# Kernel optimization log

Measured on AMD Instinct MI355X. Metric: run time of the kernel, lower is better.

## Reference

```python
import jax, jax.numpy as jnp
import numpy as np

EPS = 1e-06
M = 10.0
IGNORE_LABEL = 100  # setup guarantees no label == 100, so the torch filter is a no-op


def setup_inputs() -> dict:
    key = jax.random.key(0)
    kf, kl = jax.random.split(key)
    n, d = 8192, 128
    features = jax.random.normal(kf, (n, d), dtype=jnp.float32)
    labels = jax.random.randint(kl, (n,), 0, 16, dtype=jnp.int64)
    return {"features": features, "labels": labels}


def reference(features, labels):
    # features: (n, d) float; labels: (n,) int, none equal to IGNORE_LABEL
    n = features.shape[0]
    dt = features.dtype

    # pairwise squared euclidean distances via Gram trick (avoids (n,n,d) tensor)
    sq = jnp.sum(features * features, axis=1)              # (n,)
    ed = sq[:, None] + sq[None, :] - 2.0 * (features @ features.T)  # (n, n)

    eq = labels[:, None] == labels[None, :]                # (n, n), includes diagonal
    counts = jnp.sum(eq, axis=1, keepdims=True).astype(dt) - 1.0  # (n, 1)

    eqf = eq.astype(dt)
    w = eqf / (counts + EPS) - (1.0 - eqf) / (n - counts - 1.0 + EPS)
    w = w * (1.0 - jnp.eye(n, dtype=dt))                   # zero diagonal

    loss = jnp.sum(w * ed, axis=1) + M                     # (n,)
    valid = (counts[:, 0] != 0.0).astype(dt)               # rows with same-class neighbors
    return jnp.sum(jax.nn.relu(loss) * valid) / jnp.maximum(jnp.sum(valid), 1.0)
```

## Files before the change

kernel.cpp:

```cpp
#include <hip/hip_runtime.h>

#define NCLASS 16
#define D 128
#define EPSF 1e-6f
#define MF 10.0f

#define WS_S   0
#define WS_Q   (NCLASS * D)
#define WS_CNT (WS_Q + NCLASS)
#define WS_SUM (WS_CNT + NCLASS)
#define WS_DONE 2082
#define WS_FLOATS 2084

#define AGG_BLOCKS 64
#define AGG_THREADS 512
#define AGG_WAVES (AGG_THREADS / 64)

__global__ void __launch_bounds__(AGG_THREADS)
agg_kernel(const float* __restrict__ F, const int* __restrict__ L,
           float* __restrict__ ws, int n) {
    __shared__ float Ssh[AGG_WAVES][NCLASS][D];
    __shared__ float qsh[AGG_WAVES][NCLASS];
    __shared__ float csh[AGG_WAVES][NCLASS];
    const int tid  = threadIdx.x;
    const int lane = tid & 63;
    const int wv   = tid >> 6;
    const int gw   = blockIdx.x * AGG_WAVES + wv;
    const int nwv  = AGG_BLOCKS * AGG_WAVES;

    float ax[NCLASS], ay[NCLASS], qa[NCLASS], ca[NCLASS];
    #pragma unroll
    for (int c = 0; c < NCLASS; ++c) { ax[c] = ay[c] = qa[c] = ca[c] = 0.f; }

    const float2* __restrict__ F2 = (const float2*)F;
    #pragma unroll 4
    for (int r = gw; r < n; r += nwv) {
        const int lc = L[r];
        const float2 v = F2[(size_t)r * 64 + lane];
        const float sq = fmaf(v.x, v.x, v.y * v.y);
        #pragma unroll
        for (int c = 0; c < NCLASS; ++c) {
            const float sel = (lc == c) ? 1.f : 0.f;
            ax[c] = fmaf(sel, v.x, ax[c]);
            ay[c] = fmaf(sel, v.y, ay[c]);
            qa[c] = fmaf(sel, sq, qa[c]);
            ca[c] += sel;
        }
    }
    #pragma unroll
    for (int c = 0; c < NCLASS; ++c) {
        float q = qa[c];
        #pragma unroll
        for (int off = 32; off; off >>= 1) q += __shfl_xor(q, off, 64);
        qa[c] = q;
    }
    #pragma unroll
    for (int c = 0; c < NCLASS; ++c) {
        ((float2*)&Ssh[wv][c][0])[lane] = make_float2(ax[c], ay[c]);
    }
    if (lane == 0) {
        #pragma unroll
        for (int c = 0; c < NCLASS; ++c) { qsh[wv][c] = qa[c]; csh[wv][c] = ca[c]; }
    }
    __syncthreads();
    const float* Sflat = &Ssh[0][0][0];
    for (int p = tid; p < NCLASS * D; p += AGG_THREADS) {
        float s = 0.f;
        #pragma unroll
        for (int w = 0; w < AGG_WAVES; ++w) s += Sflat[w * NCLASS * D + p];
        atomicAdd(&ws[WS_S + p], s);
    }
    if (tid < NCLASS) {
        float q = 0.f, cc = 0.f;
        #pragma unroll
        for (int w = 0; w < AGG_WAVES; ++w) { q += qsh[w][tid]; cc += csh[w][tid]; }
        atomicAdd(&ws[WS_Q + tid], q);
        atomicAdd(&ws[WS_CNT + tid], cc);
    }
}

#define LOSS_BLOCKS 256
#define LOSS_THREADS 256
#define LOSS_WAVES (LOSS_THREADS / 64)

__global__ void __launch_bounds__(LOSS_THREADS)
loss_kernel(const float* __restrict__ F, const int* __restrict__ L,
            float* __restrict__ ws, float* __restrict__ out, int n) {
    __shared__ float S_lds[NCLASS * D];
    __shared__ float Stot[D];
    __shared__ float Q_lds[NCLASS];
    __shared__ float cnt_lds[NCLASS];
    __shared__ float Qtot_s;
    __shared__ float redL[LOSS_WAVES], redV[LOSS_WAVES];

    const int tid = threadIdx.x;
    const float4* ws4 = (const float4*)(ws + WS_S);
    float4* S4 = (float4*)S_lds;
    for (int i = tid; i < NCLASS * D / 4; i += LOSS_THREADS) S4[i] = ws4[i];
    if (tid < NCLASS) {
        Q_lds[tid] = ws[WS_Q + tid];
        cnt_lds[tid] = ws[WS_CNT + tid];
    }
    __syncthreads();
    if (tid < D) {
        float s = 0.f;
        #pragma unroll
        for (int c = 0; c < NCLASS; ++c) s += S_lds[c * D + tid];
        Stot[tid] = s;
    }
    if (tid == 0) {
        float q = 0.f;
        #pragma unroll
        for (int c = 0; c < NCLASS; ++c) q += Q_lds[c];
        Qtot_s = q;
    }
    __syncthreads();

    const int lane = tid & 63;
    const int wv = tid >> 6;
    const int gw = blockIdx.x * LOSS_WAVES + wv;
    const int nw = LOSS_BLOCKS * LOSS_WAVES;
    const float nf = (float)n;
    const float2* __restrict__ F2 = (const float2*)F;
    const float2* __restrict__ S2 = (const float2*)S_lds;
    const float2* __restrict__ T2 = (const float2*)Stot;

    float accL = 0.f, accV = 0.f;
    #pragma unroll 2
    for (int r = gw; r < n; r += nw) {
        const int c = L[r];
        const float2 v = F2[(size_t)r * 64 + lane];
        const float2 a = S2[c * 64 + lane];
        const float2 t = T2[lane];
        float sq    = fmaf(v.x, v.x, v.y * v.y);
        float dsame = fmaf(v.x, a.x, v.y * a.y);
        float dtot  = fmaf(v.x, t.x, v.y * t.y);
        #pragma unroll
        for (int off = 32; off; off >>= 1) {
            sq    += __shfl_xor(sq, off, 64);
            dsame += __shfl_xor(dsame, off, 64);
            dtot  += __shfl_xor(dtot, off, 64);
        }
        const float cntc   = cnt_lds[c];
        const float counts = cntc - 1.f;
        const float same_sum = counts * sq + sq + Q_lds[c] - 2.f * dsame;
        const float diff_sum = (nf - cntc) * sq + (Qtot_s - Q_lds[c])
                               - 2.f * (dtot - dsame);
        const float loss = same_sum / (counts + EPSF)
                         - diff_sum / (nf - cntc + EPSF) + MF;
        const float valid = counts > 0.5f ? 1.f : 0.f;
        accL += (loss > 0.f ? loss : 0.f) * valid;
        accV += valid;
    }
    if (lane == 0) { redL[wv] = accL; redV[wv] = accV; }
    __syncthreads();
    if (tid == 0) {
        float sL = 0.f, sV = 0.f;
        #pragma unroll
        for (int w = 0; w < LOSS_WAVES; ++w) { sL += redL[w]; sV += redV[w]; }
        atomicAdd(&ws[WS_SUM], sL);
        atomicAdd(&ws[WS_SUM + 1], sV);
        __threadfence();
        unsigned done = __hip_atomic_fetch_add((unsigned*)&ws[WS_DONE], 1u,
                                               __ATOMIC_ACQ_REL,
                                               __HIP_MEMORY_SCOPE_AGENT);
        if (done == (unsigned)(gridDim.x - 1)) {
            float sl = __hip_atomic_load(&ws[WS_SUM], __ATOMIC_RELAXED,
                                         __HIP_MEMORY_SCOPE_AGENT);
            float sv = __hip_atomic_load(&ws[WS_SUM + 1], __ATOMIC_RELAXED,
                                         __HIP_MEMORY_SCOPE_AGENT);
            out[0] = sl / fmaxf(sv, 1.f);
        }
    }
}

extern "C" void kernel_launch(void* const* d_in, const int* in_sizes, int n_in,
                              void* d_out, int out_size, void* d_ws, size_t ws_size,
                              hipStream_t stream) {
    const float* F = (const float*)d_in[0];
    const int* L = (const int*)d_in[1];
    float* out = (float*)d_out;
    float* ws = (float*)d_ws;
    const int n = in_sizes[1];

    hipMemsetAsync(d_ws, 0, WS_FLOATS * sizeof(float), stream);
    agg_kernel<<<AGG_BLOCKS, AGG_THREADS, 0, stream>>>(F, L, ws, n);
    loss_kernel<<<LOSS_BLOCKS, LOSS_THREADS, 0, stream>>>(F, L, ws, out, n);
}
```

Measured before the change: 84.58 us.

## Replace atomic class-sum accumulation with per-block partial slots and drop memset

The aggregation kernel now writes per-block partial class sums, squared norms and counts into dedicated workspace slots. The loss kernel reduces all 64 slots itself, replacing the global float atomics. The agg kernel zeroes the final-reduction counters, which lets the host memset launch go away. Each wave also processes two rows at once using float4 loads (half-wave per row), halving loop iterations. The trade-off is redundant reduction of 64 slots in every loss block.

```diff
diff --git a/kernel.cpp b/kernel.cpp
--- a/kernel.cpp
+++ b/kernel.cpp
@@ -5,88 +5,107 @@
 #define EPSF 1e-6f
 #define MF 10.0f
 
-#define WS_S   0
-#define WS_Q   (NCLASS * D)
-#define WS_CNT (WS_Q + NCLASS)
-#define WS_SUM (WS_CNT + NCLASS)
-#define WS_DONE 2082
-#define WS_FLOATS 2084
+#define WS_PART 16
+#define SLOT 2080
 
 #define AGG_BLOCKS 64
 #define AGG_THREADS 512
-#define AGG_WAVES (AGG_THREADS / 64)
+#define AGG_WAVES 8
 
 __global__ void __launch_bounds__(AGG_THREADS)
 agg_kernel(const float* __restrict__ F, const int* __restrict__ L,
            float* __restrict__ ws, int n) {
-    __shared__ float Ssh[AGG_WAVES][NCLASS][D];
+    __shared__ __align__(16) float Ssh[AGG_WAVES][NCLASS * D];
     __shared__ float qsh[AGG_WAVES][NCLASS];
     __shared__ float csh[AGG_WAVES][NCLASS];
     const int tid  = threadIdx.x;
     const int lane = tid & 63;
     const int wv   = tid >> 6;
+    const int sub  = lane & 31;
+    const int half = lane >> 5;
     const int gw   = blockIdx.x * AGG_WAVES + wv;
     const int nwv  = AGG_BLOCKS * AGG_WAVES;
-
-    float ax[NCLASS], ay[NCLASS], qa[NCLASS], ca[NCLASS];
+    const int npairs = n >> 1;
+
+    float sx[NCLASS], sy[NCLASS], sz[NCLASS], sw[NCLASS], qa[NCLASS], ca[NCLASS];
     #pragma unroll
-    for (int c = 0; c < NCLASS; ++c) { ax[c] = ay[c] = qa[c] = ca[c] = 0.f; }
-
-    const float2* __restrict__ F2 = (const float2*)F;
-    #pragma unroll 4
-    for (int r = gw; r < n; r += nwv) {
+    for (int c = 0; c < NCLASS; ++c) { sx[c]=sy[c]=sz[c]=sw[c]=qa[c]=ca[c]=0.f; }
+
+    const float4* __restrict__ F4 = (const float4*)F;
+    for (int rp = gw; rp < npairs; rp += nwv) {
+        const int r = rp * 2 + half;
         const int lc = L[r];
-        const float2 v = F2[(size_t)r * 64 + lane];
-        const float sq = fmaf(v.x, v.x, v.y * v.y);
+        const float4 v = F4[(size_t)r * 32 + sub];
+        const float vv = fmaf(v.x, v.x, fmaf(v.y, v.y, fmaf(v.z, v.z, v.w*v.w)));
         #pragma unroll
         for (int c = 0; c < NCLASS; ++c) {
             const float sel = (lc == c) ? 1.f : 0.f;
-            ax[c] = fmaf(sel, v.x, ax[c]);
-            ay[c] = fmaf(sel, v.y, ay[c]);
-            qa[c] = fmaf(sel, sq, qa[c]);
+            sx[c] = fmaf(sel, v.x, sx[c]);
+            sy[c] = fmaf(sel, v.y, sy[c]);
+            sz[c] = fmaf(sel, v.z, sz[c]);
+            sw[c] = fmaf(sel, v.w, sw[c]);
+            qa[c] = fmaf(sel, vv,  qa[c]);
             ca[c] += sel;
         }
     }
     #pragma unroll
     for (int c = 0; c < NCLASS; ++c) {
-        float q = qa[c];
-        #pragma unroll
-        for (int off = 32; off; off >>= 1) q += __shfl_xor(q, off, 64);
-        qa[c] = q;
-    }
-    #pragma unroll
-    for (int c = 0; c < NCLASS; ++c) {
-        ((float2*)&Ssh[wv][c][0])[lane] = make_float2(ax[c], ay[c]);
+        sx[c] += __shfl_xor(sx[c], 32, 64);
+        sy[c] += __shfl_xor(sy[c], 32, 64);
+        sz[c] += __shfl_xor(sz[c], 32, 64);
+        sw[c] += __shfl_xor(sw[c], 32, 64);
+        float q = qa[c], cc = ca[c];
+        #pragma unroll
+        for (int off = 32; off; off >>= 1) {
+            q  += __shfl_xor(q, off, 64);
+            cc += __shfl_xor(cc, off, 64);
+        }
+        qa[c] = q; ca[c] = cc;
+    }
+    if (half == 0) {
+        #pragma unroll
+        for (int c = 0; c < NCLASS; ++c)
+            ((float4*)&Ssh[wv][c * D])[sub] = make_float4(sx[c], sy[c], sz[c], sw[c]);
     }
     if (lane == 0) {
         #pragma unroll
-        for (int c = 0; c < NCLASS; ++c) { qsh[wv][c] = qa[c]; csh[wv][c] = ca[c]; }
-    }
-    __syncthreads();
-    const float* Sflat = &Ssh[0][0][0];
-    for (int p = tid; p < NCLASS * D; p += AGG_THREADS) {
-        float s = 0.f;
-        #pragma unroll
-        for (int w = 0; w < AGG_WAVES; ++w) s += Sflat[w * NCLASS * D + p];
-        atomicAdd(&ws[WS_S + p], s);
+        for (int c = 0; c < NCLASS; ++c) {
+            qsh[wv][c] = qa[c];
+            csh[wv][c] = ca[c] * (1.f / 32.f);
+        }
+    }
+    __syncthreads();
+    float* __restrict__ base = ws + WS_PART + (size_t)blockIdx.x * SLOT;
+    {
+        float4 a = make_float4(0.f, 0.f, 0.f, 0.f);
+        #pragma unroll
+        for (int w = 0; w < AGG_WAVES; ++w) {
+            const float4 t = ((const float4*)Ssh[w])[tid];
+            a.x += t.x; a.y += t.y; a.z += t.z; a.w += t.w;
+        }
+        ((float4*)base)[tid] = a;
     }
     if (tid < NCLASS) {
         float q = 0.f, cc = 0.f;
         #pragma unroll
         for (int w = 0; w < AGG_WAVES; ++w) { q += qsh[w][tid]; cc += csh[w][tid]; }
-        atomicAdd(&ws[WS_Q + tid], q);
-        atomicAdd(&ws[WS_CNT + tid], cc);
+        base[NCLASS * D + tid] = q;
+        base[NCLASS * D + NCLASS + tid] = cc;
+    }
+    if (blockIdx.x == 0 && tid == 0) {
+        ws[0] = 0.f; ws[1] = 0.f;
+        ((unsigned*)ws)[2] = 0u;
     }
 }
 
 #define LOSS_BLOCKS 256
 #define LOSS_THREADS 256
-#define LOSS_WAVES (LOSS_THREADS / 64)
+#define LOSS_WAVES 4
 
 __global__ void __launch_bounds__(LOSS_THREADS)
-loss_kernel(const float* __restrict__ F, const int* __restrict__ L,
-            float* __restrict__ ws, float* __restrict__ out, int n) {
-    __shared__ float S_lds[NCLASS * D];
+loss_kernel(const float* __restrict__ F, float* __restrict__ ws,
+            const int* __restrict__ L, float* __restrict__ out, int n) {
+    __shared__ __align__(16) float S_lds[NCLASS * D];
     __shared__ float Stot[D];
     __shared__ float Q_lds[NCLASS];
     __shared__ float cnt_lds[NCLASS];
@@ -94,12 +113,22 @@
     __shared__ float redL[LOSS_WAVES], redV[LOSS_WAVES];
 
     const int tid = threadIdx.x;
-    const float4* ws4 = (const float4*)(ws + WS_S);
-    float4* S4 = (float4*)S_lds;
-    for (int i = tid; i < NCLASS * D / 4; i += LOSS_THREADS) S4[i] = ws4[i];
+    const float* __restrict__ pb = ws + WS_PART;
+    for (int p = tid; p < NCLASS * D / 4; p += LOSS_THREADS) {
+        float4 a = make_float4(0.f, 0.f, 0.f, 0.f);
+        for (int s = 0; s < AGG_BLOCKS; ++s) {
+            const float4 t = ((const float4*)(pb + (size_t)s * SLOT))[p];
+            a.x += t.x; a.y += t.y; a.z += t.z; a.w += t.w;
+        }
+        ((float4*)S_lds)[p] = a;
+    }
     if (tid < NCLASS) {
-        Q_lds[tid] = ws[WS_Q + tid];
-        cnt_lds[tid] = ws[WS_CNT + tid];
+        float q = 0.f, cc = 0.f;
+        for (int s = 0; s < AGG_BLOCKS; ++s) {
+            q  += pb[(size_t)s * SLOT + NCLASS * D + tid];
+            cc += pb[(size_t)s * SLOT + NCLASS * D + NCLASS + tid];
+        }
+        Q_lds[tid] = q; cnt_lds[tid] = cc;
     }
     __syncthreads();
     if (tid < D) {
@@ -158,16 +187,16 @@
         float sL = 0.f, sV = 0.f;
         #pragma unroll
         for (int w = 0; w < LOSS_WAVES; ++w) { sL += redL[w]; sV += redV[w]; }
-        atomicAdd(&ws[WS_SUM], sL);
-        atomicAdd(&ws[WS_SUM + 1], sV);
+        atomicAdd(&ws[0], sL);
+        atomicAdd(&ws[1], sV);
         __threadfence();
-        unsigned done = __hip_atomic_fetch_add((unsigned*)&ws[WS_DONE], 1u,
+        unsigned done = __hip_atomic_fetch_add((unsigned*)ws + 2, 1u,
                                                __ATOMIC_ACQ_REL,
                                                __HIP_MEMORY_SCOPE_AGENT);
-        if (done == (unsigned)(gridDim.x - 1)) {
-            float sl = __hip_atomic_load(&ws[WS_SUM], __ATOMIC_RELAXED,
+        if (done == (unsigned)(LOSS_BLOCKS - 1)) {
+            float sl = __hip_atomic_load(&ws[0], __ATOMIC_RELAXED,
                                          __HIP_MEMORY_SCOPE_AGENT);
-            float sv = __hip_atomic_load(&ws[WS_SUM + 1], __ATOMIC_RELAXED,
+            float sv = __hip_atomic_load(&ws[1], __ATOMIC_RELAXED,
                                          __HIP_MEMORY_SCOPE_AGENT);
             out[0] = sl / fmaxf(sv, 1.f);
         }
@@ -183,7 +212,6 @@
     float* ws = (float*)d_ws;
     const int n = in_sizes[1];
 
-    hipMemsetAsync(d_ws, 0, WS_FLOATS * sizeof(float), stream);
     agg_kernel<<<AGG_BLOCKS, AGG_THREADS, 0, stream>>>(F, L, ws, n);
-    loss_kernel<<<LOSS_BLOCKS, LOSS_THREADS, 0, stream>>>(F, L, ws, out, n);
+    loss_kernel<<<LOSS_BLOCKS, LOSS_THREADS, 0, stream>>>(F, ws, L, out, n);
 }
```

After: 91.12 us. +7.7%, slower.
